# Kernel tuning notes

Hardware: AMD Instinct MI355X
Metric: run time of the kernel (lower is better)

Reference implementation:

```python
import jax, jax.numpy as jnp
import numpy as np

N_NODES = 100000
N_EDGES = 1600000
NODE_F = 64
EDGE_F = 32
BN_EPS = 1e-5


def setup_inputs() -> dict:
    key = jax.random.key(0)
    ks = jax.random.split(key, 8)
    in_dim = 2 * NODE_F + EDGE_F  # 160
    scale = 1.0 / np.sqrt(in_dim)
    return {
        "node_attrs": jax.random.normal(ks[0], (N_NODES, NODE_F), jnp.float32),
        "edge_index": jax.random.randint(ks[1], (2, N_EDGES), 0, N_NODES, jnp.int64),
        "edge_attrs": jax.random.normal(ks[2], (N_EDGES, EDGE_F), jnp.float32),
        "W_f": jax.random.normal(ks[3], (in_dim, NODE_F), jnp.float32) * scale,
        "b_f": jnp.zeros((NODE_F,), jnp.float32),
        "W_s": jax.random.normal(ks[4], (in_dim, NODE_F), jnp.float32) * scale,
        "b_s": jnp.zeros((NODE_F,), jnp.float32),
        "gamma": jnp.ones((NODE_F,), jnp.float32),
        "beta": jnp.zeros((NODE_F,), jnp.float32),
    }


def reference(node_attrs, edge_index, edge_attrs, W_f, b_f, W_s, b_s, gamma, beta):
    source, target = edge_index[0], edge_index[1]
    x_i = node_attrs[source]            # [E, F] gather
    x_j = node_attrs[target]            # [E, F] gather
    z = jnp.concatenate([x_i, x_j, edge_attrs], axis=-1)  # [E, 2F+Fe]
    # gated MLP: sigmoid(lin_f(z)) * softplus(lin_s(z))
    h = jax.nn.sigmoid(z @ W_f + b_f) * jax.nn.softplus(z @ W_s + b_s)  # [E, F]
    # scatter-add messages to source nodes
    message = jax.ops.segment_sum(h, source, num_segments=node_attrs.shape[0])  # [N, F]
    # BatchNorm1d in training mode: batch stats over node dim (biased variance)
    mean = jnp.mean(message, axis=0)
    var = jnp.mean((message - mean) ** 2, axis=0)
    normed = (message - mean) * jax.lax.rsqrt(var + BN_EPS) * gamma + beta
    return node_attrs + normed
```

## Files before the change

kernel.cpp:

```cpp
#include <hip/hip_runtime.h>
#include <math.h>

#define N_NODES 100000
#define N_EDGES 1600000
#define NODE_F  64
#define IN_DIM  160
#define N_TILES 25000
#define ZSTRIDE 168
#define EDGE_GRID 1536

typedef __attribute__((ext_vector_type(8))) short short8;
typedef __attribute__((ext_vector_type(4))) float f32x4;

static __device__ inline unsigned short f2bf(float f) {
    union { float f; unsigned u; } v; v.f = f;
    unsigned r = v.u + 0x7fffu + ((v.u >> 16) & 1u);
    return (unsigned short)(r >> 16);
}

static __device__ inline unsigned pack2(float lo, float hi) {
    union { float f; unsigned u; } a, b; a.f = lo; b.f = hi;
    const unsigned ra = a.u + 0x7fffu + ((a.u >> 16) & 1u);
    const unsigned rb = b.u + 0x7fffu + ((b.u >> 16) & 1u);
    return __builtin_amdgcn_perm(rb, ra, 0x07060302u);
}

__global__ __launch_bounds__(256, 6) void edge_kernel(
    const float* __restrict__ node_attrs,
    const int*   __restrict__ edge_src,
    const int*   __restrict__ edge_tgt,
    const float* __restrict__ edge_attrs,
    const float* __restrict__ W_f, const float* __restrict__ b_f,
    const float* __restrict__ W_s, const float* __restrict__ b_s,
    float* __restrict__ msg)
{
    __shared__ __align__(16) short sbuf[64 * ZSTRIDE];
    unsigned* sbuf32 = (unsigned*)sbuf;

    const int tid  = threadIdx.x;
    const int wave = tid >> 6;
    const int lane = tid & 63;
    const int quad = lane >> 4;
    const int l15  = lane & 15;

    short8 bF[5], bS[5];
#pragma unroll
    for (int mat = 0; mat < 2; ++mat) {
        const float* W = mat ? W_s : W_f;
        __syncthreads();
        for (int idx = tid; idx < IN_DIM * 64; idx += 256) {
            const int k = idx >> 6, n = idx & 63;
            sbuf[n * ZSTRIDE + k] = (short)f2bf(W[idx]);
        }
        __syncthreads();
#pragma unroll
        for (int kc = 0; kc < 5; ++kc) {
            const short8 b = *(const short8*)&sbuf[(16 * wave + l15) * ZSTRIDE + kc * 32 + quad * 8];
            if (mat) bS[kc] = b; else bF[kc] = b;
        }
    }

    const float bias_f = b_f[16 * wave + l15];
    const float bias_s = b_s[16 * wave + l15];
    float* const msgf  = msg + 16 * wave + l15;

    int srcv = edge_src[blockIdx.x * 64 + lane];
    int tgtv = edge_tgt[blockIdx.x * 64 + lane];

    for (int t = blockIdx.x; t < N_TILES; t += EDGE_GRID) {
        const int e0 = t * 64;

        __syncthreads();

#pragma unroll
        for (int i = 0; i < 8; ++i) {
            const int el   = i * 2 + (quad >> 1);
            const int half = quad & 1;
            const int sl   = 16 * wave + el;
            const int ns   = __shfl(srcv, sl);
            const int nt   = __shfl(tgtv, sl);
            const int node = half ? nt : ns;
            const float4 v = *(const float4*)&node_attrs[node * 64 + l15 * 4];
            uint2 o; o.x = pack2(v.x, v.y); o.y = pack2(v.z, v.w);
            *(uint2*)&sbuf32[sl * (ZSTRIDE / 2) + half * 32 + l15 * 2] = o;
        }
#pragma unroll
        for (int i = 0; i < 2; ++i) {
            const int p  = i * 256 + tid;
            const int el = p >> 3, g = p & 7;
            const float4 v = *(const float4*)&edge_attrs[(size_t)(e0 + el) * 32 + g * 4];
            uint2 o; o.x = pack2(v.x, v.y); o.y = pack2(v.z, v.w);
            *(uint2*)&sbuf32[el * (ZSTRIDE / 2) + 64 + g * 2] = o;
        }

        const int tn = t + EDGE_GRID;
        int nsrc = 0, ntgt = 0;
        if (tn < N_TILES) {
            nsrc = edge_src[tn * 64 + lane];
            ntgt = edge_tgt[tn * 64 + lane];
        }
        __syncthreads();

#pragma unroll
        for (int mt = 0; mt < 4; ++mt) {
            f32x4 accF = {0.f, 0.f, 0.f, 0.f};
            f32x4 accS = {0.f, 0.f, 0.f, 0.f};
#pragma unroll
            for (int kc = 0; kc < 5; ++kc) {
                const short8 a = *(const short8*)&sbuf[(mt * 16 + l15) * ZSTRIDE + kc * 32 + quad * 8];
                accF = __builtin_amdgcn_mfma_f32_16x16x32_bf16(a, bF[kc], accF, 0, 0, 0);
                accS = __builtin_amdgcn_mfma_f32_16x16x32_bf16(a, bS[kc], accS, 0, 0, 0);
            }
#pragma unroll
            for (int r = 0; r < 4; ++r) {
                const float xf = accF[r] + bias_f;
                const float xs = accS[r] + bias_s;
                const float sig = __builtin_amdgcn_rcpf(1.0f + __expf(-xf));
                const float sp  = fmaxf(xs, 0.0f) + __logf(1.0f + __expf(-fabsf(xs)));
                const float h   = sig * sp;
                const int sl    = mt * 16 + quad * 4 + r;
                const int node  = __shfl(srcv, sl);
                atomicAdd(&msgf[node * 64], h);
            }
        }

        srcv = nsrc;
        tgtv = ntgt;
    }
}

#define STATS_BLOCKS 400
__global__ __launch_bounds__(256) void stats_kernel(
    const float* __restrict__ msg, float* __restrict__ stats)
{
    const int tid = threadIdx.x;
    const int f = tid & 63;
    const int g = tid >> 6;
    float s = 0.0f, q = 0.0f;
    for (int r = blockIdx.x * 4 + g; r < N_NODES; r += STATS_BLOCKS * 4) {
        const float v = msg[r * 64 + f];
        s += v;
        q = fmaf(v, v, q);
    }
    __shared__ float rs[4][64];
    __shared__ float rq[4][64];
    rs[g][f] = s;
    rq[g][f] = q;
    __syncthreads();
    if (tid < 64) {
        const float ss = rs[0][f] + rs[1][f] + rs[2][f] + rs[3][f];
        const float qq = rq[0][f] + rq[1][f] + rq[2][f] + rq[3][f];
        atomicAdd(&stats[f], ss);
        atomicAdd(&stats[64 + f], qq);
    }
}

__global__ __launch_bounds__(256) void norm_kernel(
    const float* __restrict__ node_attrs,
    const float* __restrict__ stats,
    const float* __restrict__ gamma,
    const float* __restrict__ beta,
    float* __restrict__ out)
{
    const int i = blockIdx.x * blockDim.x + threadIdx.x;
    const int idx = i * 4;
    if (idx >= N_NODES * 64) return;
    const int f = idx & 63;
    const float inv_n = 1.0f / (float)N_NODES;

    const float4 m4 = *(const float4*)&out[idx];
    const float4 x4 = *(const float4*)&node_attrs[idx];

    float mean[4], rstd[4], gm[4], bt[4];
#pragma unroll
    for (int j = 0; j < 4; ++j) {
        mean[j] = stats[f + j] * inv_n;
        const float var = stats[64 + f + j] * inv_n - mean[j] * mean[j];
        rstd[j] = rsqrtf(var + 1e-5f);
        gm[j] = gamma[f + j];
        bt[j] = beta[f + j];
    }
    float4 o;
    o.x = x4.x + (m4.x - mean[0]) * rstd[0] * gm[0] + bt[0];
    o.y = x4.y + (m4.y - mean[1]) * rstd[1] * gm[1] + bt[1];
    o.z = x4.z + (m4.z - mean[2]) * rstd[2] * gm[2] + bt[2];
    o.w = x4.w + (m4.w - mean[3]) * rstd[3] * gm[3] + bt[3];
    *(float4*)&out[idx] = o;
}

extern "C" void kernel_launch(void* const* d_in, const int* in_sizes, int n_in,
                              void* d_out, int out_size, void* d_ws, size_t ws_size,
                              hipStream_t stream)
{
    const float* node_attrs = (const float*)d_in[0];
    const int*   edge_index = (const int*)d_in[1];
    const float* edge_attrs = (const float*)d_in[2];
    const float* W_f   = (const float*)d_in[3];
    const float* b_f   = (const float*)d_in[4];
    const float* W_s   = (const float*)d_in[5];
    const float* b_s   = (const float*)d_in[6];
    const float* gamma = (const float*)d_in[7];
    const float* beta  = (const float*)d_in[8];

    float* out   = (float*)d_out;
    float* stats = (float*)d_ws;

    const int* edge_src = edge_index;
    const int* edge_tgt = edge_index + N_EDGES;

    hipMemsetAsync(out, 0, (size_t)N_NODES * NODE_F * sizeof(float), stream);
    hipMemsetAsync(stats, 0, 128 * sizeof(float), stream);

    edge_kernel<<<EDGE_GRID, 256, 0, stream>>>(
        node_attrs, edge_src, edge_tgt, edge_attrs, W_f, b_f, W_s, b_s, out);

    stats_kernel<<<STATS_BLOCKS, 256, 0, stream>>>(out, stats);

    norm_kernel<<<(N_NODES * NODE_F / 4 + 255) / 256, 256, 0, stream>>>(
        node_attrs, stats, gamma, beta, out);
}
```

Baseline: 635.9 us.

## Sort edges by source via counting sort and merge atomics per node run

Adds a counting-sort pipeline (histogram, three-stage scan, atomic scatter) that reorders edges by source node, then a sorted edge kernel that gathers edge attributes through the permutation. Rows are permuted in LDS so each lane's accumulator rows are consecutive sorted edges, letting runs of the same source be summed in registers before one atomicAdd. This aims to cut global atomic traffic and contention. In exchange it adds several kernel launches, extra index traffic and an uncoalesced edge_attrs gather, and it depends on workspace size. With random sources (about 16 edges per node), runs inside a lane's 16 edges are short, so the atomic savings may be small.

Result: slower. 751.1 us (+18.1%).

```diff
diff --git a/kernel.cpp b/kernel.cpp
--- a/kernel.cpp
+++ b/kernel.cpp
@@ -9,6 +9,9 @@
 #define ZSTRIDE 168
 #define EDGE_GRID 1536
 
+#define SCAN_BLOCKS 391
+#define E_BLOCKS    6250
+
 typedef __attribute__((ext_vector_type(8))) short short8;
 typedef __attribute__((ext_vector_type(4))) float f32x4;
 
@@ -23,6 +26,198 @@
     const unsigned ra = a.u + 0x7fffu + ((a.u >> 16) & 1u);
     const unsigned rb = b.u + 0x7fffu + ((b.u >> 16) & 1u);
     return __builtin_amdgcn_perm(rb, ra, 0x07060302u);
+}
+
+static __device__ inline int permrow(int e) {
+    return ((e >> 2) & 3) * 16 + (e >> 4) * 4 + (e & 3);
+}
+
+__global__ __launch_bounds__(256) void hist_kernel(
+    const int* __restrict__ src, int* __restrict__ hist)
+{
+    const int e = blockIdx.x * 256 + threadIdx.x;
+    if (e < N_EDGES) atomicAdd(&hist[src[e]], 1);
+}
+
+__global__ __launch_bounds__(256) void scan1_kernel(
+    const int* __restrict__ hist, int* __restrict__ partial)
+{
+    __shared__ int lds[256];
+    const int tid = threadIdx.x;
+    const int idx = blockIdx.x * 256 + tid;
+    lds[tid] = (idx < N_NODES) ? hist[idx] : 0;
+    __syncthreads();
+    for (int s = 128; s > 0; s >>= 1) {
+        if (tid < s) lds[tid] += lds[tid + s];
+        __syncthreads();
+    }
+    if (tid == 0) partial[blockIdx.x] = lds[0];
+}
+
+__global__ __launch_bounds__(512) void scan2_kernel(int* __restrict__ partial)
+{
+    __shared__ int lds[512];
+    const int tid = threadIdx.x;
+    const int v = (tid < SCAN_BLOCKS) ? partial[tid] : 0;
+    lds[tid] = v;
+    __syncthreads();
+    for (int off = 1; off < 512; off <<= 1) {
+        const int t = (tid >= off) ? lds[tid - off] : 0;
+        __syncthreads();
+        lds[tid] += t;
+        __syncthreads();
+    }
+    if (tid < SCAN_BLOCKS) partial[tid] = lds[tid] - v;
+}
+
+__global__ __launch_bounds__(256) void scan3_kernel(
+    int* __restrict__ hist, const int* __restrict__ partial)
+{
+    __shared__ int lds[256];
+    const int tid = threadIdx.x;
+    const int idx = blockIdx.x * 256 + tid;
+    const int v = (idx < N_NODES) ? hist[idx] : 0;
+    lds[tid] = v;
+    __syncthreads();
+    for (int off = 1; off < 256; off <<= 1) {
+        const int t = (tid >= off) ? lds[tid - off] : 0;
+        __syncthreads();
+        lds[tid] += t;
+        __syncthreads();
+    }
+    if (idx < N_NODES) hist[idx] = lds[tid] - v + partial[blockIdx.x];
+}
+
+__global__ __launch_bounds__(256) void scatter_kernel(
+    const int* __restrict__ src, const int* __restrict__ tgt,
+    int* __restrict__ cursor,
+    int* __restrict__ sSrc, int* __restrict__ sTgt, int* __restrict__ perm)
+{
+    const int e = blockIdx.x * 256 + threadIdx.x;
+    if (e >= N_EDGES) return;
+    const int s = src[e];
+    const int pos = atomicAdd(&cursor[s], 1);
+    sSrc[pos] = s;
+    sTgt[pos] = tgt[e];
+    perm[pos] = e;
+}
+
+__global__ __launch_bounds__(256, 6) void edge_kernel_sorted(
+    const float* __restrict__ node_attrs,
+    const int*   __restrict__ sSrc,
+    const int*   __restrict__ sTgt,
+    const int*   __restrict__ perm,
+    const float* __restrict__ edge_attrs,
+    const float* __restrict__ W_f, const float* __restrict__ b_f,
+    const float* __restrict__ W_s, const float* __restrict__ b_s,
+    float* __restrict__ msg)
+{
+    __shared__ __align__(16) short sbuf[64 * ZSTRIDE];
+    unsigned* sbuf32 = (unsigned*)sbuf;
+
+    const int tid  = threadIdx.x;
+    const int wave = tid >> 6;
+    const int lane = tid & 63;
+    const int quad = lane >> 4;
+    const int l15  = lane & 15;
+
+    short8 bF[5], bS[5];
+#pragma unroll
+    for (int mat = 0; mat < 2; ++mat) {
+        const float* W = mat ? W_s : W_f;
+        __syncthreads();
+        for (int idx = tid; idx < IN_DIM * 64; idx += 256) {
+            const int k = idx >> 6, n = idx & 63;
+            sbuf[n * ZSTRIDE + k] = (short)f2bf(W[idx]);
+        }
+        __syncthreads();
+#pragma unroll
+        for (int kc = 0; kc < 5; ++kc) {
+            const short8 b = *(const short8*)&sbuf[(16 * wave + l15) * ZSTRIDE + kc * 32 + quad * 8];
+            if (mat) bS[kc] = b; else bF[kc] = b;
+        }
+    }
+
+    const float bias_f = b_f[16 * wave + l15];
+    const float bias_s = b_s[16 * wave + l15];
+    float* const msgf  = msg + 16 * wave + l15;
+
+    int srcv = sSrc[blockIdx.x * 64 + lane];
+    int tgtv = sTgt[blockIdx.x * 64 + lane];
+    int prmv = perm[blockIdx.x * 64 + lane];
+
+    for (int t = blockIdx.x; t < N_TILES; t += EDGE_GRID) {
+        __syncthreads();
+
+        const int tn = t + EDGE_GRID;
+        int nsrc = 0, ntgt = 0, nprm = 0;
+        if (tn < N_TILES) {
+            nsrc = sSrc[tn * 64 + lane];
+            ntgt = sTgt[tn * 64 + lane];
+            nprm = perm[tn * 64 + lane];
+        }
+
+#pragma unroll
+        for (int i = 0; i < 8; ++i) {
+            const int el   = i * 2 + (quad >> 1);
+            const int half = quad & 1;
+            const int sl   = 16 * wave + el;
+            const int ns   = __shfl(srcv, sl);
+            const int nt   = __shfl(tgtv, sl);
+            const int node = half ? nt : ns;
+            const int row  = permrow(sl);
+            const float4 v = *(const float4*)&node_attrs[node * 64 + l15 * 4];
+            uint2 o; o.x = pack2(v.x, v.y); o.y = pack2(v.z, v.w);
+            *(uint2*)&sbuf32[row * (ZSTRIDE / 2) + half * 32 + l15 * 2] = o;
+        }
+#pragma unroll
+        for (int i = 0; i < 2; ++i) {
+            const int p  = i * 256 + tid;
+            const int el = p >> 3, g = p & 7;
+            const int pe = __shfl(prmv, el);
+            const int row = permrow(el);
+            const float4 v = *(const float4*)&edge_attrs[(size_t)pe * 32 + g * 4];
+            uint2 o; o.x = pack2(v.x, v.y); o.y = pack2(v.z, v.w);
+            *(uint2*)&sbuf32[row * (ZSTRIDE / 2) + 64 + g * 2] = o;
+        }
+        __syncthreads();
+
+        int lastn = -1;
+        float carry = 0.0f;
+#pragma unroll
+        for (int mt = 0; mt < 4; ++mt) {
+            f32x4 accF = {0.f, 0.f, 0.f, 0.f};
+            f32x4 accS = {0.f, 0.f, 0.f, 0.f};
+#pragma unroll
+            for (int kc = 0; kc < 5; ++kc) {
+                const short8 a = *(const short8*)&sbuf[(mt * 16 + l15) * ZSTRIDE + kc * 32 + quad * 8];
+                accF = __builtin_amdgcn_mfma_f32_16x16x32_bf16(a, bF[kc], accF, 0, 0, 0);
+                accS = __builtin_amdgcn_mfma_f32_16x16x32_bf16(a, bS[kc], accS, 0, 0, 0);
+            }
+#pragma unroll
+            for (int r = 0; r < 4; ++r) {
+                const float xf = accF[r] + bias_f;
+                const float xs = accS[r] + bias_s;
+                const float sig = __builtin_amdgcn_rcpf(1.0f + __expf(-xf));
+                const float sp  = fmaxf(xs, 0.0f) + __logf(1.0f + __expf(-fabsf(xs)));
+                const float h   = sig * sp;
+                const int e     = quad * 16 + mt * 4 + r;
+                const int n     = __shfl(srcv, e);
+                if (n == lastn) {
+                    carry += h;
+                } else {
+                    if (lastn >= 0) atomicAdd(&msgf[lastn * 64], carry);
+                    lastn = n;
+                    carry = h;
+                }
+            }
+        }
+        atomicAdd(&msgf[lastn * 64], carry);
+
+        srcv = nsrc;
+        tgtv = ntgt;
+        prmv = nprm;
+    }
 }
 
 __global__ __launch_bounds__(256, 6) void edge_kernel(
@@ -69,9 +264,7 @@
 
     for (int t = blockIdx.x; t < N_TILES; t += EDGE_GRID) {
         const int e0 = t * 64;
-
-        __syncthreads();
-
+        __syncthreads();
 #pragma unroll
         for (int i = 0; i < 8; ++i) {
             const int el   = i * 2 + (quad >> 1);
@@ -92,7 +285,6 @@
             uint2 o; o.x = pack2(v.x, v.y); o.y = pack2(v.z, v.w);
             *(uint2*)&sbuf32[el * (ZSTRIDE / 2) + 64 + g * 2] = o;
         }
-
         const int tn = t + EDGE_GRID;
         int nsrc = 0, ntgt = 0;
         if (tn < N_TILES) {
@@ -100,7 +292,6 @@
             ntgt = edge_tgt[tn * 64 + lane];
         }
         __syncthreads();
-
 #pragma unroll
         for (int mt = 0; mt < 4; ++mt) {
             f32x4 accF = {0.f, 0.f, 0.f, 0.f};
@@ -123,7 +314,6 @@
                 atomicAdd(&msgf[node * 64], h);
             }
         }
-
         srcv = nsrc;
         tgtv = ntgt;
     }
@@ -208,11 +398,31 @@
     const int* edge_src = edge_index;
     const int* edge_tgt = edge_index + N_EDGES;
 
+    char* wsb = (char*)d_ws;
+    int* partial = (int*)(wsb + 1024);
+    int* hist    = (int*)(wsb + 4096);
+    int* perm    = (int*)(wsb + 404224);
+    int* sSrc    = perm + N_EDGES;
+    int* sTgt    = sSrc + N_EDGES;
+    const size_t WS_NEED = 404224 + 3ull * N_EDGES * 4;
+
     hipMemsetAsync(out, 0, (size_t)N_NODES * NODE_F * sizeof(float), stream);
     hipMemsetAsync(stats, 0, 128 * sizeof(float), stream);
 
-    edge_kernel<<<EDGE_GRID, 256, 0, stream>>>(
-        node_attrs, edge_src, edge_tgt, edge_attrs, W_f, b_f, W_s, b_s, out);
+    if (ws_size >= WS_NEED) {
+        hipMemsetAsync(hist, 0, (size_t)N_NODES * sizeof(int), stream);
+        hist_kernel<<<E_BLOCKS, 256, 0, stream>>>(edge_src, hist);
+        scan1_kernel<<<SCAN_BLOCKS, 256, 0, stream>>>(hist, partial);
+        scan2_kernel<<<1, 512, 0, stream>>>(partial);
+        scan3_kernel<<<SCAN_BLOCKS, 256, 0, stream>>>(hist, partial);
+        scatter_kernel<<<E_BLOCKS, 256, 0, stream>>>(
+            edge_src, edge_tgt, hist, sSrc, sTgt, perm);
+        edge_kernel_sorted<<<EDGE_GRID, 256, 0, stream>>>(
+            node_attrs, sSrc, sTgt, perm, edge_attrs, W_f, b_f, W_s, b_s, out);
+    } else {
+        edge_kernel<<<EDGE_GRID, 256, 0, stream>>>(
+            node_attrs, edge_src, edge_tgt, edge_attrs, W_f, b_f, W_s, b_s, out);
+    }
 
     stats_kernel<<<STATS_BLOCKS, 256, 0, stream>>>(out, stats);
 
```

## Precompute per-node linear projections and gather them per edge

Applied to the files above, without the earlier changes.

Splits the concatenated-input matmul algebraically: node_attrs times the source and target slices of W_f/W_s are computed once per node into PS/QT workspace tables (interleaved f/s columns). The edge kernel then only does the 32-wide edge-attribute matmul and adds gathered per-node projections before the gated activation and scatter-add. This cuts per-edge MFMA work and LDS staging of 128 gathered node features, at the cost of an extra precompute pass and gathering 128-float rows (two float2 per lane) from a ~100MB workspace. The old path is kept as a fallback when the workspace is too small.

New measurement: 716.2 us. 12.6% more time.

```diff
diff --git a/kernel.cpp b/kernel.cpp
--- a/kernel.cpp
+++ b/kernel.cpp
@@ -8,6 +8,9 @@
 #define N_TILES 25000
 #define ZSTRIDE 168
 #define EDGE_GRID 1536
+#define PQ_GRID  2048
+#define PRE_GRID 512
+#define PRE_TILES 1563
 
 typedef __attribute__((ext_vector_type(8))) short short8;
 typedef __attribute__((ext_vector_type(4))) float f32x4;
@@ -23,6 +26,165 @@
     const unsigned ra = a.u + 0x7fffu + ((a.u >> 16) & 1u);
     const unsigned rb = b.u + 0x7fffu + ((b.u >> 16) & 1u);
     return __builtin_amdgcn_perm(rb, ra, 0x07060302u);
+}
+
+__global__ __launch_bounds__(256, 3) void precompute_kernel(
+    const float* __restrict__ X,
+    const float* __restrict__ W_f, const float* __restrict__ W_s,
+    float* __restrict__ PS, float* __restrict__ QT)
+{
+    __shared__ __align__(16) short wtps[128 * 68];
+    __shared__ __align__(16) short wtqt[128 * 68];
+    __shared__ __align__(16) short xl[64 * 72];
+    unsigned* xl32 = (unsigned*)xl;
+
+    const int tid  = threadIdx.x;
+    const int wave = tid >> 6;
+    const int lane = tid & 63;
+    const int quad = lane >> 4;
+    const int l15  = lane & 15;
+
+    for (int idx = tid; idx < 128 * 64; idx += 256) {
+        const int c = idx >> 6;
+        const int k = idx & 63;
+        const int j = c >> 1;
+        const float* W = (c & 1) ? W_s : W_f;
+        wtps[c * 68 + k] = (short)f2bf(W[k * 64 + j]);
+        wtqt[c * 68 + k] = (short)f2bf(W[(k + 64) * 64 + j]);
+    }
+    __syncthreads();
+
+    const short* wt = (wave >> 1) ? wtqt : wtps;
+    const int colbase = (wave & 1) * 64;
+    float* const OUT = (wave >> 1) ? QT : PS;
+
+    short8 bfr[4][2];
+#pragma unroll
+    for (int nt = 0; nt < 4; ++nt)
+#pragma unroll
+        for (int kc = 0; kc < 2; ++kc)
+            bfr[nt][kc] = *(const short8*)&wt[(colbase + nt * 16 + l15) * 68 + kc * 32 + quad * 8];
+
+    for (int t = blockIdx.x; t < PRE_TILES; t += PRE_GRID) {
+        const int n0 = t * 64;
+        __syncthreads();
+        for (int idx = tid; idx < 64 * 16; idx += 256) {
+            const int row = idx >> 4, c4 = idx & 15;
+            float4 v = {0.f, 0.f, 0.f, 0.f};
+            if (n0 + row < N_NODES)
+                v = *(const float4*)&X[(size_t)(n0 + row) * 64 + c4 * 4];
+            uint2 o; o.x = pack2(v.x, v.y); o.y = pack2(v.z, v.w);
+            *(uint2*)&xl32[row * 36 + c4 * 2] = o;
+        }
+        __syncthreads();
+
+#pragma unroll
+        for (int mt = 0; mt < 4; ++mt) {
+            short8 a0 = *(const short8*)&xl[(mt * 16 + l15) * 72 + 0 * 32 + quad * 8];
+            short8 a1 = *(const short8*)&xl[(mt * 16 + l15) * 72 + 1 * 32 + quad * 8];
+#pragma unroll
+            for (int nt = 0; nt < 4; ++nt) {
+                f32x4 acc = {0.f, 0.f, 0.f, 0.f};
+                acc = __builtin_amdgcn_mfma_f32_16x16x32_bf16(a0, bfr[nt][0], acc, 0, 0, 0);
+                acc = __builtin_amdgcn_mfma_f32_16x16x32_bf16(a1, bfr[nt][1], acc, 0, 0, 0);
+#pragma unroll
+                for (int r = 0; r < 4; ++r) {
+                    const int node = n0 + mt * 16 + quad * 4 + r;
+                    if (node < N_NODES)
+                        OUT[(size_t)node * 128 + colbase + nt * 16 + l15] = acc[r];
+                }
+            }
+        }
+    }
+}
+
+__global__ __launch_bounds__(256, 8) void edge_pq_kernel(
+    const float* __restrict__ PS,
+    const float* __restrict__ QT,
+    const int*   __restrict__ edge_src,
+    const int*   __restrict__ edge_tgt,
+    const float* __restrict__ edge_attrs,
+    const float* __restrict__ W_f, const float* __restrict__ b_f,
+    const float* __restrict__ W_s, const float* __restrict__ b_s,
+    float* __restrict__ msg)
+{
+    __shared__ __align__(16) short ebuf[64 * 40];
+    __shared__ __align__(16) short wet[64 * 72];
+
+    const int tid  = threadIdx.x;
+    const int wave = tid >> 6;
+    const int lane = tid & 63;
+    const int quad = lane >> 4;
+    const int l15  = lane & 15;
+
+    for (int idx = tid; idx < 64 * 32; idx += 256) {
+        const int c = idx >> 5, k = idx & 31;
+        wet[c * 72 + k]      = (short)f2bf(W_f[(k + 128) * 64 + c]);
+        wet[c * 72 + 32 + k] = (short)f2bf(W_s[(k + 128) * 64 + c]);
+    }
+    __syncthreads();
+    const short8 bFe = *(const short8*)&wet[(16 * wave + l15) * 72 + quad * 8];
+    const short8 bSe = *(const short8*)&wet[(16 * wave + l15) * 72 + 32 + quad * 8];
+
+    const float bias_f = b_f[16 * wave + l15];
+    const float bias_s = b_s[16 * wave + l15];
+    const int   fcol2  = 2 * (16 * wave + l15);
+    float* const msgf  = msg + 16 * wave + l15;
+
+    const int sel = tid >> 2;
+    const int sg  = tid & 3;
+
+    int srcv = edge_src[blockIdx.x * 64 + lane];
+    int tgtv = edge_tgt[blockIdx.x * 64 + lane];
+
+    for (int t = blockIdx.x; t < N_TILES; t += PQ_GRID) {
+        const int e0 = t * 64;
+
+        __syncthreads();
+
+        {
+            const float4 v0 = *(const float4*)&edge_attrs[(size_t)(e0 + sel) * 32 + sg * 8];
+            const float4 v1 = *(const float4*)&edge_attrs[(size_t)(e0 + sel) * 32 + sg * 8 + 4];
+            short8 o;
+            unsigned* o32 = (unsigned*)&o;
+            o32[0] = pack2(v0.x, v0.y); o32[1] = pack2(v0.z, v0.w);
+            o32[2] = pack2(v1.x, v1.y); o32[3] = pack2(v1.z, v1.w);
+            *(short8*)&ebuf[sel * 40 + sg * 8] = o;
+        }
+
+        const int tn = t + PQ_GRID;
+        int nsrc = 0, ntgt = 0;
+        if (tn < N_TILES) {
+            nsrc = edge_src[tn * 64 + lane];
+            ntgt = edge_tgt[tn * 64 + lane];
+        }
+        __syncthreads();
+
+#pragma unroll
+        for (int mt = 0; mt < 4; ++mt) {
+            const short8 a = *(const short8*)&ebuf[(mt * 16 + l15) * 40 + quad * 8];
+            f32x4 accF = {0.f, 0.f, 0.f, 0.f};
+            f32x4 accS = {0.f, 0.f, 0.f, 0.f};
+            accF = __builtin_amdgcn_mfma_f32_16x16x32_bf16(a, bFe, accF, 0, 0, 0);
+            accS = __builtin_amdgcn_mfma_f32_16x16x32_bf16(a, bSe, accS, 0, 0, 0);
+#pragma unroll
+            for (int r = 0; r < 4; ++r) {
+                const int e = mt * 16 + quad * 4 + r;
+                const int s = __shfl(srcv, e);
+                const int g = __shfl(tgtv, e);
+                const float2 ps = *(const float2*)&PS[(size_t)s * 128 + fcol2];
+                const float2 qt = *(const float2*)&QT[(size_t)g * 128 + fcol2];
+                const float xf = accF[r] + ps.x + qt.x + bias_f;
+                const float xs = accS[r] + ps.y + qt.y + bias_s;
+                const float sig = __builtin_amdgcn_rcpf(1.0f + __expf(-xf));
+                const float sp  = fmaxf(xs, 0.0f) + __logf(1.0f + __expf(-fabsf(xs)));
+                atomicAdd(&msgf[s * 64], sig * sp);
+            }
+        }
+
+        srcv = nsrc;
+        tgtv = ntgt;
+    }
 }
 
 __global__ __launch_bounds__(256, 6) void edge_kernel(
@@ -69,9 +231,7 @@
 
     for (int t = blockIdx.x; t < N_TILES; t += EDGE_GRID) {
         const int e0 = t * 64;
-
-        __syncthreads();
-
+        __syncthreads();
 #pragma unroll
         for (int i = 0; i < 8; ++i) {
             const int el   = i * 2 + (quad >> 1);
@@ -92,7 +252,6 @@
             uint2 o; o.x = pack2(v.x, v.y); o.y = pack2(v.z, v.w);
             *(uint2*)&sbuf32[el * (ZSTRIDE / 2) + 64 + g * 2] = o;
         }
-
         const int tn = t + EDGE_GRID;
         int nsrc = 0, ntgt = 0;
         if (tn < N_TILES) {
@@ -100,7 +259,6 @@
             ntgt = edge_tgt[tn * 64 + lane];
         }
         __syncthreads();
-
 #pragma unroll
         for (int mt = 0; mt < 4; ++mt) {
             f32x4 accF = {0.f, 0.f, 0.f, 0.f};
@@ -123,7 +281,6 @@
                 atomicAdd(&msgf[node * 64], h);
             }
         }
-
         srcv = nsrc;
         tgtv = ntgt;
     }
@@ -205,14 +362,24 @@
     float* out   = (float*)d_out;
     float* stats = (float*)d_ws;
 
+    float* PS = (float*)((char*)d_ws + 4096);
+    float* QT = PS + (size_t)N_NODES * 128;
+    const size_t WS_NEED = 4096 + 2ull * N_NODES * 128 * sizeof(float);
+
     const int* edge_src = edge_index;
     const int* edge_tgt = edge_index + N_EDGES;
 
     hipMemsetAsync(out, 0, (size_t)N_NODES * NODE_F * sizeof(float), stream);
     hipMemsetAsync(stats, 0, 128 * sizeof(float), stream);
 
-    edge_kernel<<<EDGE_GRID, 256, 0, stream>>>(
-        node_attrs, edge_src, edge_tgt, edge_attrs, W_f, b_f, W_s, b_s, out);
+    if (ws_size >= WS_NEED) {
+        precompute_kernel<<<PRE_GRID, 256, 0, stream>>>(node_attrs, W_f, W_s, PS, QT);
+        edge_pq_kernel<<<PQ_GRID, 256, 0, stream>>>(
+            PS, QT, edge_src, edge_tgt, edge_attrs, W_f, b_f, W_s, b_s, out);
+    } else {
+        edge_kernel<<<EDGE_GRID, 256, 0, stream>>>(
+            node_attrs, edge_src, edge_tgt, edge_attrs, W_f, b_f, W_s, b_s, out);
+    }
 
     stats_kernel<<<STATS_BLOCKS, 256, 0, stream>>>(out, stats);
 
```
